# Performance work log

Measured on AMD Instinct MI355X. Metric: run time of the kernel, lower is better.

The kernel has to match this reference:

```python
import jax, jax.numpy as jnp
import numpy as np

DILATED_K = 3  # init kwarg dilated_parameter_k -> 2**k = 8


def setup_inputs() -> dict:
    key = jax.random.key(0)
    k1, k2, k3, k4 = jax.random.split(key, 4)
    B, H, R, F = 16, 8, 400, 256
    A = jax.random.uniform(k1, (B, H, R, R), dtype=jnp.float32)
    feats = jax.random.normal(k2, (B, H, R, F), dtype=jnp.float32)
    # Linear(features, features) params (torch layout: weight [out, in], bias [out])
    lim = 1.0 / np.sqrt(F)
    W = jax.random.uniform(k3, (F, F), dtype=jnp.float32, minval=-lim, maxval=lim)
    b = jax.random.uniform(k4, (F,), dtype=jnp.float32, minval=-lim, maxval=lim)
    return {"Adjancy_Matrix": A, "features": feats, "W": W, "b": b}


def reference(Adjancy_Matrix, features, W, b):
    # Deterministic reference: takes the prob < 0.8 (dilated) branch of the
    # original module (the other branch is pure random dropout of the mask).
    two_k = 2 ** DILATED_K  # 8
    # torch.sort(A, descending=True, dim=3).indices == argsort of -A along last dim
    idx = jnp.argsort(-Adjancy_Matrix, axis=3)  # [B,H,R,R] int32
    # mask = 1 where sorted column index is 0 or in {2^k, ..., 2^k+4}
    mask = (idx == 0) | ((idx >= two_k) & (idx <= two_k + 4))
    R = Adjancy_Matrix.shape[2]
    mask = mask | jnp.eye(R, dtype=bool)  # add identity per (b, h), clamp >=1 -> 1
    masked_A = Adjancy_Matrix * mask.astype(Adjancy_Matrix.dtype)
    agg = jnp.einsum('bhij,bhjf->bhif', masked_A, features)  # [B,H,R,F]
    out = jax.nn.relu(agg @ W.T + b)
    return out + features
```

## Files before the change

kernel.cpp:

```cpp
#include <hip/hip_runtime.h>

typedef unsigned short u16;
typedef unsigned int   u32;
typedef unsigned long long u64;
typedef __bf16 bf16x8 __attribute__((ext_vector_type(8)));
typedef float  f32x4  __attribute__((ext_vector_type(4)));
typedef u32    u32x4  __attribute__((ext_vector_type(4)));
typedef u16    u16x4  __attribute__((ext_vector_type(4)));
typedef u16    u16x8v __attribute__((ext_vector_type(8)));

#define R_DIM 400
#define F_DIM 256
#define M_TOT 51200

__device__ __forceinline__ u16 f2bf(float f) {
    union { float f; u32 i; } x; x.f = f;
    u32 r = x.i + 0x7FFFu + ((x.i >> 16) & 1u);
    return (u16)(r >> 16);
}

__global__ __launch_bounds__(256) void wprep_f32(const float* __restrict__ W,
                                                 u16* __restrict__ Wf) {
    int g  = blockIdx.x * 256 + threadIdx.x;
    int ks = g >> 10;
    int T  = (g >> 6) & 15;
    int L  = g & 63;
    int n  = T * 16 + (L & 15);
    int k  = ks * 32 + (L >> 4) * 8;
    const float* wp = W + (size_t)n * F_DIM + k;
    float4 lo = *(const float4*)wp;
    float4 hi = *(const float4*)(wp + 4);
    u16x8v t;
    t[0] = f2bf(lo.x); t[1] = f2bf(lo.y); t[2] = f2bf(lo.z); t[3] = f2bf(lo.w);
    t[4] = f2bf(hi.x); t[5] = f2bf(hi.y); t[6] = f2bf(hi.z); t[7] = f2bf(hi.w);
    *(u16x8v*)(Wf + (size_t)g * 8) = t;
}

__device__ __forceinline__ void compute_slots(float4 v0, float4 v1r, int lane,
                                              int row, u32 es[7], u32* dup_out) {
    float4 v1 = v1r;
    if (lane >= 36) { v1.x = -1.f; v1.y = -1.f; v1.z = -1.f; v1.w = -1.f; }
    float refs[6];
    refs[0] = __shfl(v0.x, 0);
    refs[1] = __shfl(v0.x, 2);
    refs[2] = __shfl(v0.y, 2);
    refs[3] = __shfl(v0.z, 2);
    refs[4] = __shfl(v0.w, 2);
    refs[5] = __shfl(v0.x, 3);
    const int cols[6] = {0, 8, 9, 10, 11, 12};
    float e0[4] = {v0.x, v0.y, v0.z, v0.w};
    float e1[4] = {v1.x, v1.y, v1.z, v1.w};
    u32 cnt[6];
#pragma unroll
    for (int k = 0; k < 6; k++) {
        int c = 0;
#pragma unroll
        for (int jj = 0; jj < 4; jj++) {
            int j = (lane << 2) + jj;
            c += __popcll(__ballot(e0[jj] > refs[k] ||
                                   (e0[jj] == refs[k] && j < cols[k])));
            c += __popcll(__ballot(e1[jj] > refs[k]));
        }
        cnt[k] = (u32)c;
    }
    int i = row % R_DIM;
    bool dup = (i == (int)cnt[0]) | (i == (int)cnt[1]) | (i == (int)cnt[2]) |
               (i == (int)cnt[3]) | (i == (int)cnt[4]) | (i == (int)cnt[5]);
#pragma unroll
    for (int s = 0; s < 6; s++) es[s] = cnt[s];
    es[6] = (u32)i;
    *dup_out = dup ? 1u : 0u;
}

__global__ __launch_bounds__(256) void gcn_fused(const float* __restrict__ A,
                                                 const float* __restrict__ feats,
                                                 const u16*  __restrict__ Wf,
                                                 const float* __restrict__ bias,
                                                 float* __restrict__ out) {
    __shared__ __align__(16) u16 agg_lds[32][264];
    __shared__ __align__(16) u16 probeA[16][32];
    __shared__ __align__(16) u16 probeB[16][32];

    const int tid = threadIdx.x, wid = tid >> 6, lane = tid & 63;
    const int bid = (int)blockIdx.x;
    const int m0  = ((bid & 7) * 200 + (bid >> 3)) * 32;
    const int kg  = (lane >> 4) << 3;

    for (int e = tid; e < 512; e += 256) {
        int r = e >> 5, k = e & 31;
        probeA[r][k] = (k == 0) ? f2bf((float)r) : ((k == 1) ? f2bf(1.0f) : (u16)0);
        probeB[r][k] = (k == 0) ? f2bf(16.0f)    : ((k == 1) ? f2bf((float)r) : (u16)0);
    }

    const int rbase = wid * 8;

    {
        const float* Ar0 = A + (size_t)(m0 + rbase) * R_DIM;
        float4 pa0 = *(const float4*)(Ar0 + lane * 4);
        float4 pa1 = *(const float4*)(Ar0 + (lane < 36 ? 256 + lane * 4 : 0));

        float  w_p[7];
        float4 f_p[7];
        u32    dup_p = 0;

#pragma unroll
        for (int rr = 0; rr < 8; rr++) {
            const int r   = rbase + rr;
            const int row = m0 + r;
            float4 v0 = pa0, v1 = pa1;
            if (rr < 7) {
                const float* An = A + (size_t)(row + 1) * R_DIM;
                pa0 = *(const float4*)(An + lane * 4);
                pa1 = *(const float4*)(An + (lane < 36 ? 256 + lane * 4 : 0));
            }

            u32 es[7], dupm;
            compute_slots(v0, v1, lane, row, es, &dupm);

            const int bh = row / R_DIM;
            const float* Ar = A + (size_t)row * R_DIM;
            const float* fb = feats + (size_t)bh * R_DIM * F_DIM + lane * 4;

            float w[7]; float4 f[7];
#pragma unroll
            for (int s = 0; s < 7; s++) {
                u32 e = es[s];
                w[s] = Ar[e];
                f[s] = *(const float4*)(fb + (size_t)e * F_DIM);
            }

            if (rr > 0) {
                float a0 = 0.f, a1 = 0.f, a2 = 0.f, a3 = 0.f;
#pragma unroll
                for (int s = 0; s < 7; s++) {
                    float ws = (s == 6 && dup_p) ? 0.f : w_p[s];
                    a0 += ws * f_p[s].x; a1 += ws * f_p[s].y;
                    a2 += ws * f_p[s].z; a3 += ws * f_p[s].w;
                }
                u16x4 st = { f2bf(a0), f2bf(a1), f2bf(a2), f2bf(a3) };
                *(u16x4*)&agg_lds[r - 1][lane * 4] = st;
            }
#pragma unroll
            for (int s = 0; s < 7; s++) { w_p[s] = w[s]; f_p[s] = f[s]; }
            dup_p = dupm;
        }
        {
            float a0 = 0.f, a1 = 0.f, a2 = 0.f, a3 = 0.f;
#pragma unroll
            for (int s = 0; s < 7; s++) {
                float ws = (s == 6 && dup_p) ? 0.f : w_p[s];
                a0 += ws * f_p[s].x; a1 += ws * f_p[s].y;
                a2 += ws * f_p[s].z; a3 += ws * f_p[s].w;
            }
            u16x4 st = { f2bf(a0), f2bf(a1), f2bf(a2), f2bf(a3) };
            *(u16x4*)&agg_lds[rbase + 7][lane * 4] = st;
        }
    }
    __syncthreads();

    int rowi[4], coli[4];
    {
        bf16x8 pa = *(const bf16x8*)&probeA[lane & 15][kg];
        bf16x8 pb = *(const bf16x8*)&probeB[lane & 15][kg];
        f32x4 pd = {0.f, 0.f, 0.f, 0.f};
        pd = __builtin_amdgcn_mfma_f32_16x16x32_bf16(pa, pb, pd, 0, 0, 0);
#pragma unroll
        for (int reg = 0; reg < 4; reg++) {
            int v = (int)(pd[reg] + 0.5f);
            rowi[reg] = v >> 4;
            coli[reg] = v & 15;
        }
    }

    f32x4 acc[2][4];
#pragma unroll
    for (int mt = 0; mt < 2; mt++)
#pragma unroll
        for (int nt = 0; nt < 4; nt++)
            acc[mt][nt] = (f32x4){0.f, 0.f, 0.f, 0.f};

    for (int ks = 0; ks < 8; ks++) {
        bf16x8 af[2], bfr[4];
#pragma unroll
        for (int mt = 0; mt < 2; mt++)
            af[mt] = *(const bf16x8*)&agg_lds[mt * 16 + (lane & 15)][ks * 32 + kg];
#pragma unroll
        for (int nt = 0; nt < 4; nt++) {
            int T = wid * 4 + nt;
            u32x4 v = *(const u32x4*)(Wf + ((size_t)(ks * 16 + T) * 64 + lane) * 8);
            bfr[nt] = __builtin_bit_cast(bf16x8, v);
        }
#pragma unroll
        for (int mt = 0; mt < 2; mt++)
#pragma unroll
            for (int nt = 0; nt < 4; nt++)
                acc[mt][nt] = __builtin_amdgcn_mfma_f32_16x16x32_bf16(
                    af[mt], bfr[nt], acc[mt][nt], 0, 0, 0);
    }

#pragma unroll
    for (int nt = 0; nt < 4; nt++) {
        int nb = wid * 64 + nt * 16;
#pragma unroll
        for (int reg = 0; reg < 4; reg++) {
            int gn = nb + coli[reg];
            float bn = bias[gn];
#pragma unroll
            for (int mt = 0; mt < 2; mt++) {
                int gm = m0 + mt * 16 + rowi[reg];
                size_t off = (size_t)gm * F_DIM + gn;
                out[off] = fmaxf(acc[mt][nt][reg] + bn, 0.f) + feats[off];
            }
        }
    }
}

extern "C" void kernel_launch(void* const* d_in, const int* in_sizes, int n_in,
                              void* d_out, int out_size, void* d_ws, size_t ws_size,
                              hipStream_t stream) {
    const float* A     = (const float*)d_in[0];
    const float* feats = (const float*)d_in[1];
    const float* W     = (const float*)d_in[2];
    const float* bias  = (const float*)d_in[3];
    float* out = (float*)d_out;

    u16* Wf = (u16*)d_ws;

    wprep_f32<<<32, 256, 0, stream>>>(W, Wf);
    gcn_fused<<<M_TOT / 32, 256, 0, stream>>>(A, feats, Wf, bias, out);
}
```

Before: 215.3 us.

## Switch to single-wave blocks of 16 rows with deeper gather prefetch

Each block becomes one 64-lane wave that handles 16 rows and computes all 16 N-tiles of the output GEMM itself. This removes the block-wide __syncthreads. Row loads now run two rows ahead through a 3-slot rotating buffer instead of one row ahead, and the batch/row index math is hoisted out of the loop. In exchange, each wave reloads the full W fragment set from global memory per block, and the larger accumulator and prefetch arrays raise register pressure, which may limit occupancy despite the launch-bounds hint.

```diff
diff --git a/kernel.cpp b/kernel.cpp
--- a/kernel.cpp
+++ b/kernel.cpp
@@ -37,7 +37,7 @@
 }
 
 __device__ __forceinline__ void compute_slots(float4 v0, float4 v1r, int lane,
-                                              int row, u32 es[7], u32* dup_out) {
+                                              int diag, u32 es[7], u32* dup_out) {
     float4 v1 = v1r;
     if (lane >= 36) { v1.x = -1.f; v1.y = -1.f; v1.z = -1.f; v1.w = -1.f; }
     float refs[6];
@@ -63,100 +63,99 @@
         }
         cnt[k] = (u32)c;
     }
-    int i = row % R_DIM;
-    bool dup = (i == (int)cnt[0]) | (i == (int)cnt[1]) | (i == (int)cnt[2]) |
-               (i == (int)cnt[3]) | (i == (int)cnt[4]) | (i == (int)cnt[5]);
+    bool dup = (diag == (int)cnt[0]) | (diag == (int)cnt[1]) | (diag == (int)cnt[2]) |
+               (diag == (int)cnt[3]) | (diag == (int)cnt[4]) | (diag == (int)cnt[5]);
 #pragma unroll
     for (int s = 0; s < 6; s++) es[s] = cnt[s];
-    es[6] = (u32)i;
+    es[6] = (u32)diag;
     *dup_out = dup ? 1u : 0u;
 }
 
-__global__ __launch_bounds__(256) void gcn_fused(const float* __restrict__ A,
-                                                 const float* __restrict__ feats,
-                                                 const u16*  __restrict__ Wf,
-                                                 const float* __restrict__ bias,
-                                                 float* __restrict__ out) {
-    __shared__ __align__(16) u16 agg_lds[32][264];
+__global__ __launch_bounds__(64, 3) void gcn_fused(const float* __restrict__ A,
+                                                   const float* __restrict__ feats,
+                                                   const u16*  __restrict__ Wf,
+                                                   const float* __restrict__ bias,
+                                                   float* __restrict__ out) {
+    __shared__ __align__(16) u16 agg_lds[16][264];
     __shared__ __align__(16) u16 probeA[16][32];
     __shared__ __align__(16) u16 probeB[16][32];
 
-    const int tid = threadIdx.x, wid = tid >> 6, lane = tid & 63;
+    const int lane = threadIdx.x & 63;
     const int bid = (int)blockIdx.x;
-    const int m0  = ((bid & 7) * 200 + (bid >> 3)) * 32;
+    const int m0  = ((bid & 7) * 400 + (bid >> 3)) * 16;
     const int kg  = (lane >> 4) << 3;
-
-    for (int e = tid; e < 512; e += 256) {
+    const int bh  = m0 / R_DIM;
+    const int i0  = m0 - bh * R_DIM;
+
+    for (int e = lane; e < 512; e += 64) {
         int r = e >> 5, k = e & 31;
         probeA[r][k] = (k == 0) ? f2bf((float)r) : ((k == 1) ? f2bf(1.0f) : (u16)0);
         probeB[r][k] = (k == 0) ? f2bf(16.0f)    : ((k == 1) ? f2bf((float)r) : (u16)0);
     }
 
-    const int rbase = wid * 8;
+    const float* Ab = A + (size_t)m0 * R_DIM;
+    const float* fb = feats + (size_t)bh * R_DIM * F_DIM + lane * 4;
 
     {
-        const float* Ar0 = A + (size_t)(m0 + rbase) * R_DIM;
-        float4 pa0 = *(const float4*)(Ar0 + lane * 4);
-        float4 pa1 = *(const float4*)(Ar0 + (lane < 36 ? 256 + lane * 4 : 0));
-
-        float  w_p[7];
-        float4 f_p[7];
-        u32    dup_p = 0;
-
-#pragma unroll
-        for (int rr = 0; rr < 8; rr++) {
-            const int r   = rbase + rr;
-            const int row = m0 + r;
-            float4 v0 = pa0, v1 = pa1;
-            if (rr < 7) {
-                const float* An = A + (size_t)(row + 1) * R_DIM;
-                pa0 = *(const float4*)(An + lane * 4);
-                pa1 = *(const float4*)(An + (lane < 36 ? 256 + lane * 4 : 0));
+        float4 a0b[3], a1b[3];
+        float  wb[3][7];
+        float4 fbv[3][7];
+        u32    dupb[3];
+
+#pragma unroll
+        for (int p = 0; p < 2; p++) {
+            const float* Ar = Ab + (size_t)p * R_DIM;
+            a0b[p] = *(const float4*)(Ar + lane * 4);
+            a1b[p] = *(const float4*)(Ar + (lane < 36 ? 256 + lane * 4 : 0));
+        }
+
+#pragma unroll
+        for (int rr = 0; rr < 16; rr++) {
+            if (rr + 2 < 16) {
+                const float* An = Ab + (size_t)(rr + 2) * R_DIM;
+                a0b[(rr + 2) % 3] = *(const float4*)(An + lane * 4);
+                a1b[(rr + 2) % 3] = *(const float4*)(An + (lane < 36 ? 256 + lane * 4 : 0));
             }
 
             u32 es[7], dupm;
-            compute_slots(v0, v1, lane, row, es, &dupm);
-
-            const int bh = row / R_DIM;
-            const float* Ar = A + (size_t)row * R_DIM;
-            const float* fb = feats + (size_t)bh * R_DIM * F_DIM + lane * 4;
-
-            float w[7]; float4 f[7];
+            compute_slots(a0b[rr % 3], a1b[rr % 3], lane, i0 + rr, es, &dupm);
+            dupb[rr % 3] = dupm;
+
+            const float* Ar = Ab + (size_t)rr * R_DIM;
 #pragma unroll
             for (int s = 0; s < 7; s++) {
                 u32 e = es[s];
-                w[s] = Ar[e];
-                f[s] = *(const float4*)(fb + (size_t)e * F_DIM);
-            }
-
-            if (rr > 0) {
+                wb[rr % 3][s]  = Ar[e];
+                fbv[rr % 3][s] = *(const float4*)(fb + (size_t)e * F_DIM);
+            }
+
+            if (rr >= 2) {
+                const int rc = rr - 2, bi = rc % 3;
                 float a0 = 0.f, a1 = 0.f, a2 = 0.f, a3 = 0.f;
 #pragma unroll
                 for (int s = 0; s < 7; s++) {
-                    float ws = (s == 6 && dup_p) ? 0.f : w_p[s];
-                    a0 += ws * f_p[s].x; a1 += ws * f_p[s].y;
-                    a2 += ws * f_p[s].z; a3 += ws * f_p[s].w;
+                    float ws = (s == 6 && dupb[bi]) ? 0.f : wb[bi][s];
+                    a0 += ws * fbv[bi][s].x; a1 += ws * fbv[bi][s].y;
+                    a2 += ws * fbv[bi][s].z; a3 += ws * fbv[bi][s].w;
                 }
                 u16x4 st = { f2bf(a0), f2bf(a1), f2bf(a2), f2bf(a3) };
-                *(u16x4*)&agg_lds[r - 1][lane * 4] = st;
-            }
-#pragma unroll
-            for (int s = 0; s < 7; s++) { w_p[s] = w[s]; f_p[s] = f[s]; }
-            dup_p = dupm;
-        }
-        {
+                *(u16x4*)&agg_lds[rc][lane * 4] = st;
+            }
+        }
+#pragma unroll
+        for (int rc = 14; rc < 16; rc++) {
+            const int bi = rc % 3;
             float a0 = 0.f, a1 = 0.f, a2 = 0.f, a3 = 0.f;
 #pragma unroll
             for (int s = 0; s < 7; s++) {
-                float ws = (s == 6 && dup_p) ? 0.f : w_p[s];
-                a0 += ws * f_p[s].x; a1 += ws * f_p[s].y;
-                a2 += ws * f_p[s].z; a3 += ws * f_p[s].w;
+                float ws = (s == 6 && dupb[bi]) ? 0.f : wb[bi][s];
+                a0 += ws * fbv[bi][s].x; a1 += ws * fbv[bi][s].y;
+                a2 += ws * fbv[bi][s].z; a3 += ws * fbv[bi][s].w;
             }
             u16x4 st = { f2bf(a0), f2bf(a1), f2bf(a2), f2bf(a3) };
-            *(u16x4*)&agg_lds[rbase + 7][lane * 4] = st;
-        }
-    }
-    __syncthreads();
+            *(u16x4*)&agg_lds[rc][lane * 4] = st;
+        }
+    }
 
     int rowi[4], coli[4];
     {
@@ -172,45 +171,31 @@
         }
     }
 
-    f32x4 acc[2][4];
-#pragma unroll
-    for (int mt = 0; mt < 2; mt++)
-#pragma unroll
-        for (int nt = 0; nt < 4; nt++)
-            acc[mt][nt] = (f32x4){0.f, 0.f, 0.f, 0.f};
-
+    f32x4 acc[16];
+#pragma unroll
+    for (int nt = 0; nt < 16; nt++) acc[nt] = (f32x4){0.f, 0.f, 0.f, 0.f};
+
+#pragma unroll
     for (int ks = 0; ks < 8; ks++) {
-        bf16x8 af[2], bfr[4];
-#pragma unroll
-        for (int mt = 0; mt < 2; mt++)
-            af[mt] = *(const bf16x8*)&agg_lds[mt * 16 + (lane & 15)][ks * 32 + kg];
-#pragma unroll
-        for (int nt = 0; nt < 4; nt++) {
-            int T = wid * 4 + nt;
-            u32x4 v = *(const u32x4*)(Wf + ((size_t)(ks * 16 + T) * 64 + lane) * 8);
-            bfr[nt] = __builtin_bit_cast(bf16x8, v);
-        }
-#pragma unroll
-        for (int mt = 0; mt < 2; mt++)
-#pragma unroll
-            for (int nt = 0; nt < 4; nt++)
-                acc[mt][nt] = __builtin_amdgcn_mfma_f32_16x16x32_bf16(
-                    af[mt], bfr[nt], acc[mt][nt], 0, 0, 0);
-    }
-
-#pragma unroll
-    for (int nt = 0; nt < 4; nt++) {
-        int nb = wid * 64 + nt * 16;
+        bf16x8 af = *(const bf16x8*)&agg_lds[lane & 15][ks * 32 + kg];
+#pragma unroll
+        for (int nt = 0; nt < 16; nt++) {
+            u32x4 v = *(const u32x4*)(Wf + ((size_t)(ks * 16 + nt) * 64 + lane) * 8);
+            bf16x8 b = __builtin_bit_cast(bf16x8, v);
+            acc[nt] = __builtin_amdgcn_mfma_f32_16x16x32_bf16(af, b, acc[nt], 0, 0, 0);
+        }
+    }
+
+#pragma unroll
+    for (int nt = 0; nt < 16; nt++) {
+        int nb = nt * 16;
 #pragma unroll
         for (int reg = 0; reg < 4; reg++) {
             int gn = nb + coli[reg];
             float bn = bias[gn];
-#pragma unroll
-            for (int mt = 0; mt < 2; mt++) {
-                int gm = m0 + mt * 16 + rowi[reg];
-                size_t off = (size_t)gm * F_DIM + gn;
-                out[off] = fmaxf(acc[mt][nt][reg] + bn, 0.f) + feats[off];
-            }
+            int gm = m0 + rowi[reg];
+            size_t off = (size_t)gm * F_DIM + gn;
+            out[off] = fmaxf(acc[nt][reg] + bn, 0.f) + feats[off];
         }
     }
 }
@@ -227,5 +212,5 @@
     u16* Wf = (u16*)d_ws;
 
     wprep_f32<<<32, 256, 0, stream>>>(W, Wf);
-    gcn_fused<<<M_TOT / 32, 256, 0, stream>>>(A, feats, Wf, bias, out);
-}
+    gcn_fused<<<M_TOT / 16, 64, 0, stream>>>(A, feats, Wf, bias, out);
+}
```

Result: slower. 253.6 us (+17.8%).

## Stage gathered feature rows into LDS via async global_load_lds with deeper prefetch

Applied to the files above, without the earlier changes.

Replaces register-held gathered feature rows with asynchronous global-to-LDS loads into a per-wave double-buffered staging area, using manual vmcnt waits to overlap the gather for one row with the accumulation of the previous row. The A-row prefetch depth grows from one row ahead to two, and the GEMM k-loop is fully unrolled. This is meant to hide gather latency and cut register pressure, at the cost of about 57 KB of extra LDS per block, which lowers occupancy. The hand-counted waitcnt values are fragile and could be wrong.

```diff
diff --git a/kernel.cpp b/kernel.cpp
--- a/kernel.cpp
+++ b/kernel.cpp
@@ -12,6 +12,14 @@
 #define R_DIM 400
 #define F_DIM 256
 #define M_TOT 51200
+
+#define VMWAIT(n) do { \
+    asm volatile("s_waitcnt vmcnt(" #n ")" ::: "memory"); \
+    __builtin_amdgcn_sched_barrier(0); \
+} while (0)
+
+typedef const __attribute__((address_space(1))) void* gvp;
+typedef __attribute__((address_space(3)))       void* lvp;
 
 __device__ __forceinline__ u16 f2bf(float f) {
     union { float f; u32 i; } x; x.f = f;
@@ -37,7 +45,7 @@
 }
 
 __device__ __forceinline__ void compute_slots(float4 v0, float4 v1r, int lane,
-                                              int row, u32 es[7], u32* dup_out) {
+                                              int diag, u32 es[7], u32* dup_out) {
     float4 v1 = v1r;
     if (lane >= 36) { v1.x = -1.f; v1.y = -1.f; v1.z = -1.f; v1.w = -1.f; }
     float refs[6];
@@ -63,12 +71,11 @@
         }
         cnt[k] = (u32)c;
     }
-    int i = row % R_DIM;
-    bool dup = (i == (int)cnt[0]) | (i == (int)cnt[1]) | (i == (int)cnt[2]) |
-               (i == (int)cnt[3]) | (i == (int)cnt[4]) | (i == (int)cnt[5]);
+    bool dup = (diag == (int)cnt[0]) | (diag == (int)cnt[1]) | (diag == (int)cnt[2]) |
+               (diag == (int)cnt[3]) | (diag == (int)cnt[4]) | (diag == (int)cnt[5]);
 #pragma unroll
     for (int s = 0; s < 6; s++) es[s] = cnt[s];
-    es[6] = (u32)i;
+    es[6] = (u32)diag;
     *dup_out = dup ? 1u : 0u;
 }
 
@@ -77,9 +84,10 @@
                                                  const u16*  __restrict__ Wf,
                                                  const float* __restrict__ bias,
                                                  float* __restrict__ out) {
-    __shared__ __align__(16) u16 agg_lds[32][264];
-    __shared__ __align__(16) u16 probeA[16][32];
-    __shared__ __align__(16) u16 probeB[16][32];
+    __shared__ __align__(16) u16   agg_lds[32][264];
+    __shared__ __align__(16) float stage[4][2][7][256];
+    __shared__ __align__(16) u16   probeA[16][32];
+    __shared__ __align__(16) u16   probeB[16][32];
 
     const int tid = threadIdx.x, wid = tid >> 6, lane = tid & 63;
     const int bid = (int)blockIdx.x;
@@ -95,62 +103,69 @@
     const int rbase = wid * 8;
 
     {
-        const float* Ar0 = A + (size_t)(m0 + rbase) * R_DIM;
-        float4 pa0 = *(const float4*)(Ar0 + lane * 4);
-        float4 pa1 = *(const float4*)(Ar0 + (lane < 36 ? 256 + lane * 4 : 0));
-
-        float  w_p[7];
-        float4 f_p[7];
-        u32    dup_p = 0;
+        float4 a0b[3], a1b[3];
+        float  wb[2][7];
+        u32    dupb[2];
+
+#pragma unroll
+        for (int p = 0; p < 2; p++) {
+            const float* Ar = A + (size_t)(m0 + rbase + p) * R_DIM;
+            a0b[p] = *(const float4*)(Ar + lane * 4);
+            a1b[p] = *(const float4*)(Ar + (lane < 36 ? 256 + lane * 4 : 0));
+        }
 
 #pragma unroll
         for (int rr = 0; rr < 8; rr++) {
             const int r   = rbase + rr;
             const int row = m0 + r;
-            float4 v0 = pa0, v1 = pa1;
-            if (rr < 7) {
-                const float* An = A + (size_t)(row + 1) * R_DIM;
-                pa0 = *(const float4*)(An + lane * 4);
-                pa1 = *(const float4*)(An + (lane < 36 ? 256 + lane * 4 : 0));
+            const int bh  = row / R_DIM;
+            const int dia = row - bh * R_DIM;
+
+            if (rr + 2 < 8) {
+                const float* An = A + (size_t)(row + 2) * R_DIM;
+                a0b[(rr + 2) % 3] = *(const float4*)(An + lane * 4);
+                a1b[(rr + 2) % 3] = *(const float4*)(An + (lane < 36 ? 256 + lane * 4 : 0));
             }
 
             u32 es[7], dupm;
-            compute_slots(v0, v1, lane, row, es, &dupm);
-
-            const int bh = row / R_DIM;
+            compute_slots(a0b[rr % 3], a1b[rr % 3], lane, dia, es, &dupm);
+            dupb[rr & 1] = dupm;
+
             const float* Ar = A + (size_t)row * R_DIM;
             const float* fb = feats + (size_t)bh * R_DIM * F_DIM + lane * 4;
-
-            float w[7]; float4 f[7];
-#pragma unroll
-            for (int s = 0; s < 7; s++) {
-                u32 e = es[s];
-                w[s] = Ar[e];
-                f[s] = *(const float4*)(fb + (size_t)e * F_DIM);
-            }
-
-            if (rr > 0) {
+#pragma unroll
+            for (int s = 0; s < 7; s++) wb[rr & 1][s] = Ar[es[s]];
+#pragma unroll
+            for (int s = 0; s < 7; s++)
+                __builtin_amdgcn_global_load_lds(
+                    (gvp)(fb + (size_t)es[s] * F_DIM),
+                    (lvp)&stage[wid][rr & 1][s][0], 16, 0, 0);
+
+            if (rr >= 1) {
+                if (rr < 6) { VMWAIT(9); } else { VMWAIT(7); }
+                const int bi = (rr - 1) & 1;
+                const float* sb = &stage[wid][bi][0][lane * 4];
                 float a0 = 0.f, a1 = 0.f, a2 = 0.f, a3 = 0.f;
 #pragma unroll
                 for (int s = 0; s < 7; s++) {
-                    float ws = (s == 6 && dup_p) ? 0.f : w_p[s];
-                    a0 += ws * f_p[s].x; a1 += ws * f_p[s].y;
-                    a2 += ws * f_p[s].z; a3 += ws * f_p[s].w;
+                    float4 f = *(const float4*)(sb + s * 256);
+                    float ws = (s == 6 && dupb[bi]) ? 0.f : wb[bi][s];
+                    a0 += ws * f.x; a1 += ws * f.y; a2 += ws * f.z; a3 += ws * f.w;
                 }
                 u16x4 st = { f2bf(a0), f2bf(a1), f2bf(a2), f2bf(a3) };
                 *(u16x4*)&agg_lds[r - 1][lane * 4] = st;
             }
-#pragma unroll
-            for (int s = 0; s < 7; s++) { w_p[s] = w[s]; f_p[s] = f[s]; }
-            dup_p = dupm;
         }
         {
+            VMWAIT(0);
+            const int bi = 7 & 1;
+            const float* sb = &stage[wid][bi][0][lane * 4];
             float a0 = 0.f, a1 = 0.f, a2 = 0.f, a3 = 0.f;
 #pragma unroll
             for (int s = 0; s < 7; s++) {
-                float ws = (s == 6 && dup_p) ? 0.f : w_p[s];
-                a0 += ws * f_p[s].x; a1 += ws * f_p[s].y;
-                a2 += ws * f_p[s].z; a3 += ws * f_p[s].w;
+                float4 f = *(const float4*)(sb + s * 256);
+                float ws = (s == 6 && dupb[bi]) ? 0.f : wb[bi][s];
+                a0 += ws * f.x; a1 += ws * f.y; a2 += ws * f.z; a3 += ws * f.w;
             }
             u16x4 st = { f2bf(a0), f2bf(a1), f2bf(a2), f2bf(a3) };
             *(u16x4*)&agg_lds[rbase + 7][lane * 4] = st;
@@ -179,6 +194,7 @@
         for (int nt = 0; nt < 4; nt++)
             acc[mt][nt] = (f32x4){0.f, 0.f, 0.f, 0.f};
 
+#pragma unroll
     for (int ks = 0; ks < 8; ks++) {
         bf16x8 af[2], bfr[4];
 #pragma unroll
```

Result: slower. 231.4 us (+7.5%).
